# Kernel optimization log

Measured on AMD Instinct MI355X. Metric: run time of the kernel, lower is better.

Reference implementation:

```python
import jax, jax.numpy as jnp
import numpy as np

DIM = 1024
SEQ = 32768
BATCH = 1
MIN_ACTIVE = 0.01
MAX_ACTIVE = 0.1
KMAX = int(MAX_ACTIVE * DIM) + 1  # static upper bound on dynamic k (<= 102)
EPS = 1e-6


def setup_inputs() -> dict:
    key = jax.random.key(0)
    ks = jax.random.split(key, 7)
    h = DIM // 8
    s = 0.02
    return {
        "x": jax.random.normal(ks[0], (BATCH, SEQ, DIM), jnp.float32),
        # complexity_net: Linear(dim, dim//8) -> GELU -> Linear(dim//8, 1) -> Sigmoid
        "w1": jax.random.normal(ks[1], (DIM, h), jnp.float32) * s,
        "b1": jnp.zeros((h,), jnp.float32),
        "w2": jax.random.normal(ks[2], (h, 1), jnp.float32) * s,
        "b2": jnp.zeros((1,), jnp.float32),
        # gate_net: Linear(dim, dim)
        "wg": jax.random.normal(ks[3], (DIM, DIM), jnp.float32) * s,
        "bg": jnp.zeros((DIM,), jnp.float32),
        # running stats (eval mode: used for normalization, not updated)
        "running_mean": jax.random.normal(ks[4], (DIM,), jnp.float32) * 0.1,
        "running_var": jax.random.uniform(ks[5], (DIM,), jnp.float32, minval=0.5, maxval=1.5),
    }


def reference(x, w1, b1, w2, b2, wg, bg, running_mean, running_var):
    # complexity from seq-mean pooled features -> scalar in (0,1)
    pooled = x.mean(axis=1, keepdims=True)                      # (B,1,D)
    hid = jax.nn.gelu(pooled @ w1 + b1, approximate=False)      # torch GELU is exact erf
    complexity = jax.nn.sigmoid(hid @ w2 + b2)                  # (B,1,1)
    active_ratio = MIN_ACTIVE + (MAX_ACTIVE - MIN_ACTIVE) * complexity
    # torch .int() truncates; clamp(min=1). B==1 so k is effectively scalar.
    k = jnp.clip((active_ratio * DIM).astype(jnp.int32), 1, KMAX)  # (B,1,1)

    importance = jnp.abs(x @ wg + bg)                           # (B,S,D)
    importance = (importance - running_mean) / (jnp.sqrt(running_var) + EPS)

    # dynamic-k topk via static-KMAX top_k + threshold at the k-th largest value
    topk_vals, _ = jax.lax.top_k(importance, KMAX)              # (B,S,KMAX)
    idx = jnp.broadcast_to((k - 1).astype(jnp.int32), (x.shape[0], x.shape[1], 1))
    kth = jnp.take_along_axis(topk_vals, idx, axis=-1)          # (B,S,1)
    mask = (importance >= kth).astype(x.dtype)                  # (B,S,D), non-differentiable
    mask = jax.lax.stop_gradient(mask)

    # straight-through combine: forward = x*mask, backward passes grad to all of x
    sparse_x = x * mask + (x - jax.lax.stop_gradient(x)) * (1.0 - mask)

    complexity_mean = complexity.mean()
    active_ratio_mean = active_ratio.mean()
    active_neurons = k.astype(jnp.float32).mean()
    return sparse_x, complexity_mean, active_ratio_mean, active_neurons
```

## Files before the change

kernel.cpp:

```cpp
#include <hip/hip_runtime.h>
#include <cstdint>
#include <cstddef>

#define SEQ 32768
#define DIM 1024
#define HID 128
#define KMAXV 103

using f4 = __attribute__((ext_vector_type(4))) float;
using f2 = __attribute__((ext_vector_type(2))) float;

__global__ __launch_bounds__(256) void pool_partial(const float* __restrict__ x,
                                                    double* __restrict__ part) {
    const int b = blockIdx.x;
    const int t = threadIdx.x;
    const int r0 = b * 128;
    double s0 = 0.0, s1 = 0.0, s2 = 0.0, s3 = 0.0;
    for (int r = 0; r < 128; ++r) {
        const float* row = x + (size_t)(r0 + r) * DIM;
        s0 += (double)row[t];
        s1 += (double)row[t + 256];
        s2 += (double)row[t + 512];
        s3 += (double)row[t + 768];
    }
    double* p = part + (size_t)b * DIM;
    p[t] = s0; p[t + 256] = s1; p[t + 512] = s2; p[t + 768] = s3;
}

__global__ __launch_bounds__(1024) void tiny_net(const double* __restrict__ part,
                                                 const float* __restrict__ w1,
                                                 const float* __restrict__ b1,
                                                 const float* __restrict__ w2,
                                                 const float* __restrict__ b2,
                                                 float* __restrict__ out_scalars,
                                                 int* __restrict__ kout) {
    __shared__ double pooled[DIM];
    __shared__ double hidv[HID];
    const int t = threadIdx.x;

    double s = 0.0;
    for (int b = 0; b < 256; ++b) s += part[(size_t)b * DIM + t];
    pooled[t] = s / (double)SEQ;
    __syncthreads();

    if (t < HID) {
        double h = (double)b1[t];
        for (int d = 0; d < DIM; ++d) h += pooled[d] * (double)w1[d * HID + t];
        h = 0.5 * h * (1.0 + erf(h * 0.70710678118654752440));
        hidv[t] = h;
    }
    __syncthreads();

    if (t == 0) {
        double z = (double)b2[0];
        for (int j = 0; j < HID; ++j) z += hidv[j] * (double)w2[j];
        double c = 1.0 / (1.0 + exp(-z));
        double ar = 0.01 + 0.09 * c;
        int k = (int)(ar * (double)DIM);
        if (k < 1) k = 1;
        if (k > KMAXV) k = KMAXV;
        out_scalars[0] = (float)c;
        out_scalars[1] = (float)ar;
        out_scalars[2] = (float)k;
        *kout = k;
    }
}

#define BM 16
#define CBLOCK 512

template<int K0, int K1>
__device__ __forceinline__ void panel_acc(const float* __restrict__ x,
                                          const float* __restrict__ wbase,
                                          int row0, float pacc[16][2]) {
#pragma unroll
    for (int m = 0; m < 16; ++m) { pacc[m][0] = 0.0f; pacc[m][1] = 0.0f; }

    f2 wc0 = *(const f2*)(wbase + (size_t)(K0 + 0) * DIM);
    f2 wc1 = *(const f2*)(wbase + (size_t)(K0 + 1) * DIM);
    f2 wc2 = *(const f2*)(wbase + (size_t)(K0 + 2) * DIM);
    f2 wc3 = *(const f2*)(wbase + (size_t)(K0 + 3) * DIM);
    f2 wn0 = *(const f2*)(wbase + (size_t)(K0 + 4) * DIM);
    f2 wn1 = *(const f2*)(wbase + (size_t)(K0 + 5) * DIM);
    f2 wn2_ = *(const f2*)(wbase + (size_t)(K0 + 6) * DIM);
    f2 wn3 = *(const f2*)(wbase + (size_t)(K0 + 7) * DIM);

    for (int kk0 = K0; kk0 < K1; kk0 += 4) {
        const int kp = kk0 + 8;
        const int kn2 = (kp < K1) ? kp : K0;
        const f2 p0 = *(const f2*)(wbase + (size_t)(kn2 + 0) * DIM);
        const f2 p1 = *(const f2*)(wbase + (size_t)(kn2 + 1) * DIM);
        const f2 p2 = *(const f2*)(wbase + (size_t)(kn2 + 2) * DIM);
        const f2 p3 = *(const f2*)(wbase + (size_t)(kn2 + 3) * DIM);

        const float* xp = x + (size_t)row0 * DIM + kk0;
#pragma unroll
        for (int m = 0; m < 16; ++m) {
            const f4 xq = *(const f4*)(xp + m * DIM);
            float a0 = pacc[m][0], a1 = pacc[m][1];
            a0 = fmaf(xq[0], wc0[0], a0); a1 = fmaf(xq[0], wc0[1], a1);
            a0 = fmaf(xq[1], wc1[0], a0); a1 = fmaf(xq[1], wc1[1], a1);
            a0 = fmaf(xq[2], wc2[0], a0); a1 = fmaf(xq[2], wc2[1], a1);
            a0 = fmaf(xq[3], wc3[0], a0); a1 = fmaf(xq[3], wc3[1], a1);
            pacc[m][0] = a0; pacc[m][1] = a1;
        }
        wc0 = wn0; wc1 = wn1; wc2 = wn2_; wc3 = wn3;
        wn0 = p0;  wn1 = p1;  wn2_ = p2;  wn3 = p3;
    }
}

__global__ __launch_bounds__(CBLOCK) void panel1_kernel(const float* __restrict__ x,
                                                        const float* __restrict__ wg,
                                                        float* __restrict__ out) {
    const int t = threadIdx.x;
    const int c2 = t << 1;
    const int row0 = blockIdx.x * BM;

    float pacc[16][2];
    panel_acc<0, 384>(x, wg + c2, row0, pacc);

#pragma unroll
    for (int m = 0; m < 16; ++m) {
        f2 v; v[0] = pacc[m][0]; v[1] = pacc[m][1];
        *(f2*)(out + (size_t)(row0 + m) * DIM + c2) = v;
    }
}

__global__ __launch_bounds__(CBLOCK) void panel23_kernel(const float* __restrict__ x,
                                                         const float* __restrict__ wg,
                                                         const float* __restrict__ bg,
                                                         const float* __restrict__ rm,
                                                         const float* __restrict__ rv,
                                                         const int* __restrict__ kptr,
                                                         float* __restrict__ out) {
    __shared__ float lbuf[8 * DIM];

    const int t = threadIdx.x;
    const int c2 = t << 1;
    const int row0 = blockIdx.x * BM;

    float pacc[16][2];

    panel_acc<384, 704>(x, wg + c2, row0, pacc);
    float d12[16][2];
#pragma unroll
    for (int m = 0; m < 16; ++m) {
        const f2 d = *(const f2*)(out + (size_t)(row0 + m) * DIM + c2);
        d12[m][0] = d[0] + pacc[m][0];
        d12[m][1] = d[1] + pacc[m][1];
    }

    panel_acc<704, 1024>(x, wg + c2, row0, pacc);
    float dot[16][2];
#pragma unroll
    for (int m = 0; m < 16; ++m) {
        dot[m][0] = d12[m][0] + pacc[m][0];
        dot[m][1] = d12[m][1] + pacc[m][1];
    }

    const f2 vbg = *(const f2*)(bg + c2);
    const f2 vrm = *(const f2*)(rm + c2);
    const f2 vrv = *(const f2*)(rv + c2);
    f2 vden;
    vden[0] = sqrtf(vrv[0]) + 1e-6f;
    vden[1] = sqrtf(vrv[1]) + 1e-6f;

    f2 imp[16];
#pragma unroll
    for (int m = 0; m < 16; ++m) {
        imp[m][0] = (fabsf(dot[m][0] + vbg[0]) - vrm[0]) / vden[0];
        imp[m][1] = (fabsf(dot[m][1] + vbg[1]) - vrm[1]) / vden[1];
    }

    int kval = *kptr;
    if (kval < 1) kval = 1;
    if (kval > DIM) kval = DIM;

    float (*selbuf)[DIM] = (float (*)[DIM])lbuf;

    for (int ch = 0; ch < 2; ++ch) {
        __syncthreads();
#pragma unroll
        for (int m = 0; m < 8; ++m)
            *(f2*)(&selbuf[m][c2]) = imp[ch * 8 + m];
        __syncthreads();

        const int w = t >> 6;
        const int l = t & 63;
        const size_t srow = (size_t)(row0 + ch * 8 + w);

        unsigned keys[16];
#pragma unroll
        for (int j = 0; j < 4; ++j) {
            const f4 v = *(const f4*)(&selbuf[w][4 * l + 256 * j]);
#pragma unroll
            for (int i = 0; i < 4; ++i) {
                const unsigned u = __float_as_uint(v[i]);
                keys[j * 4 + i] = (u & 0x80000000u) ? ~u : (u | 0x80000000u);
            }
        }

        unsigned pref = 0u;
        for (int b = 31; b >= 0; --b) {
            const unsigned tt = pref | (1u << b);
            int cnt = 0;
#pragma unroll
            for (int j = 0; j < 16; ++j) cnt += (keys[j] >= tt) ? 1 : 0;
#pragma unroll
            for (int off = 32; off >= 1; off >>= 1) cnt += __shfl_xor(cnt, off, 64);
            if (cnt >= kval) pref = tt;
        }

        const float* xr = x + srow * DIM;
        float* orow = out + srow * DIM;
#pragma unroll
        for (int j = 0; j < 4; ++j) {
            const f4 xv = *(const f4*)(xr + 4 * l + 256 * j);
            f4 o;
#pragma unroll
            for (int i = 0; i < 4; ++i) o[i] = (keys[j * 4 + i] >= pref) ? xv[i] : 0.0f;
            *(f4*)(orow + 4 * l + 256 * j) = o;
        }
    }
}

extern "C" void kernel_launch(void* const* d_in, const int* in_sizes, int n_in,
                              void* d_out, int out_size, void* d_ws, size_t ws_size,
                              hipStream_t stream) {
    const float* x  = (const float*)d_in[0];
    const float* w1 = (const float*)d_in[1];
    const float* b1 = (const float*)d_in[2];
    const float* w2 = (const float*)d_in[3];
    const float* b2 = (const float*)d_in[4];
    const float* wg = (const float*)d_in[5];
    const float* bg = (const float*)d_in[6];
    const float* rm = (const float*)d_in[7];
    const float* rv = (const float*)d_in[8];
    float* out = (float*)d_out;

    double* part = (double*)d_ws;
    int* kptr = (int*)((char*)d_ws + (size_t)256 * DIM * sizeof(double));

    pool_partial<<<256, 256, 0, stream>>>(x, part);
    tiny_net<<<1, 1024, 0, stream>>>(part, w1, b1, w2, b2,
                                     out + (size_t)SEQ * DIM, kptr);
    panel1_kernel<<<SEQ / BM, CBLOCK, 0, stream>>>(x, wg, out);
    panel23_kernel<<<SEQ / BM, CBLOCK, 0, stream>>>(x, wg, bg, rm, rv, kptr, out);
}
```

Before: 1.045 ms.

## Use packed FP32 FMA inline asm and split panel kernel into three launches

Replaces scalar fmaf accumulation with v_pk_fma_f32 inline assembly that uses scalar-register x operands broadcast across two output columns, and restructures the weight prefetch into an 8-wide double step. The former combined panel2/3 kernel is split into separate panel2 and panel3 kernels. Panel2 adds its partial into the output buffer, which panel3 then reads back. The packed FMA is meant to halve the FMA instruction count. The split is meant to cut register pressure, which should help occupancy. In exchange it adds a kernel launch and an extra read-modify-write pass over the output.

```diff
diff --git a/kernel.cpp b/kernel.cpp
--- a/kernel.cpp
+++ b/kernel.cpp
@@ -69,43 +69,55 @@
 #define BM 16
 #define CBLOCK 512
 
+__device__ __forceinline__ void fma_step(const float* __restrict__ xp,
+                                         f2 w0, f2 w1, f2 w2, f2 w3,
+                                         f2 acc[16]) {
+#pragma unroll
+    for (int m = 0; m < 16; ++m) {
+        const f2 xab = *(const f2*)(xp + m * DIM);
+        const f2 xcd = *(const f2*)(xp + m * DIM + 2);
+        asm("v_pk_fma_f32 %0, %1, %2, %0 op_sel:[0,0,0] op_sel_hi:[0,1,1]"
+            : "+v"(acc[m]) : "s"(xab), "v"(w0));
+        asm("v_pk_fma_f32 %0, %1, %2, %0 op_sel:[1,0,0] op_sel_hi:[1,1,1]"
+            : "+v"(acc[m]) : "s"(xab), "v"(w1));
+        asm("v_pk_fma_f32 %0, %1, %2, %0 op_sel:[0,0,0] op_sel_hi:[0,1,1]"
+            : "+v"(acc[m]) : "s"(xcd), "v"(w2));
+        asm("v_pk_fma_f32 %0, %1, %2, %0 op_sel:[1,0,0] op_sel_hi:[1,1,1]"
+            : "+v"(acc[m]) : "s"(xcd), "v"(w3));
+    }
+}
+
 template<int K0, int K1>
 __device__ __forceinline__ void panel_acc(const float* __restrict__ x,
                                           const float* __restrict__ wbase,
-                                          int row0, float pacc[16][2]) {
-#pragma unroll
-    for (int m = 0; m < 16; ++m) { pacc[m][0] = 0.0f; pacc[m][1] = 0.0f; }
-
-    f2 wc0 = *(const f2*)(wbase + (size_t)(K0 + 0) * DIM);
-    f2 wc1 = *(const f2*)(wbase + (size_t)(K0 + 1) * DIM);
-    f2 wc2 = *(const f2*)(wbase + (size_t)(K0 + 2) * DIM);
-    f2 wc3 = *(const f2*)(wbase + (size_t)(K0 + 3) * DIM);
-    f2 wn0 = *(const f2*)(wbase + (size_t)(K0 + 4) * DIM);
-    f2 wn1 = *(const f2*)(wbase + (size_t)(K0 + 5) * DIM);
-    f2 wn2_ = *(const f2*)(wbase + (size_t)(K0 + 6) * DIM);
-    f2 wn3 = *(const f2*)(wbase + (size_t)(K0 + 7) * DIM);
-
-    for (int kk0 = K0; kk0 < K1; kk0 += 4) {
-        const int kp = kk0 + 8;
-        const int kn2 = (kp < K1) ? kp : K0;
-        const f2 p0 = *(const f2*)(wbase + (size_t)(kn2 + 0) * DIM);
-        const f2 p1 = *(const f2*)(wbase + (size_t)(kn2 + 1) * DIM);
-        const f2 p2 = *(const f2*)(wbase + (size_t)(kn2 + 2) * DIM);
-        const f2 p3 = *(const f2*)(wbase + (size_t)(kn2 + 3) * DIM);
-
-        const float* xp = x + (size_t)row0 * DIM + kk0;
-#pragma unroll
-        for (int m = 0; m < 16; ++m) {
-            const f4 xq = *(const f4*)(xp + m * DIM);
-            float a0 = pacc[m][0], a1 = pacc[m][1];
-            a0 = fmaf(xq[0], wc0[0], a0); a1 = fmaf(xq[0], wc0[1], a1);
-            a0 = fmaf(xq[1], wc1[0], a0); a1 = fmaf(xq[1], wc1[1], a1);
-            a0 = fmaf(xq[2], wc2[0], a0); a1 = fmaf(xq[2], wc2[1], a1);
-            a0 = fmaf(xq[3], wc3[0], a0); a1 = fmaf(xq[3], wc3[1], a1);
-            pacc[m][0] = a0; pacc[m][1] = a1;
-        }
-        wc0 = wn0; wc1 = wn1; wc2 = wn2_; wc3 = wn3;
-        wn0 = p0;  wn1 = p1;  wn2_ = p2;  wn3 = p3;
+                                          int row0, f2 acc[16]) {
+#pragma unroll
+    for (int m = 0; m < 16; ++m) { acc[m][0] = 0.0f; acc[m][1] = 0.0f; }
+
+    const float* xbase = x + (size_t)row0 * DIM;
+
+    f2 a0 = *(const f2*)(wbase + (size_t)(K0 + 0) * DIM);
+    f2 a1 = *(const f2*)(wbase + (size_t)(K0 + 1) * DIM);
+    f2 a2 = *(const f2*)(wbase + (size_t)(K0 + 2) * DIM);
+    f2 a3 = *(const f2*)(wbase + (size_t)(K0 + 3) * DIM);
+
+    for (int kk0 = K0; kk0 < K1; kk0 += 8) {
+        const f2 b0 = *(const f2*)(wbase + (size_t)(kk0 + 4) * DIM);
+        const f2 b1 = *(const f2*)(wbase + (size_t)(kk0 + 5) * DIM);
+        const f2 b2v = *(const f2*)(wbase + (size_t)(kk0 + 6) * DIM);
+        const f2 b3 = *(const f2*)(wbase + (size_t)(kk0 + 7) * DIM);
+
+        fma_step(xbase + kk0, a0, a1, a2, a3, acc);
+
+        const int kn = (kk0 + 8 < K1) ? kk0 + 8 : K0;
+        const f2 c0 = *(const f2*)(wbase + (size_t)(kn + 0) * DIM);
+        const f2 c1 = *(const f2*)(wbase + (size_t)(kn + 1) * DIM);
+        const f2 c2v = *(const f2*)(wbase + (size_t)(kn + 2) * DIM);
+        const f2 c3 = *(const f2*)(wbase + (size_t)(kn + 3) * DIM);
+
+        fma_step(xbase + kk0 + 4, b0, b1, b2v, b3, acc);
+
+        a0 = c0; a1 = c1; a2 = c2v; a3 = c3;
     }
 }
 
@@ -116,46 +128,56 @@
     const int c2 = t << 1;
     const int row0 = blockIdx.x * BM;
 
-    float pacc[16][2];
+    f2 pacc[16];
     panel_acc<0, 384>(x, wg + c2, row0, pacc);
 
 #pragma unroll
-    for (int m = 0; m < 16; ++m) {
-        f2 v; v[0] = pacc[m][0]; v[1] = pacc[m][1];
-        *(f2*)(out + (size_t)(row0 + m) * DIM + c2) = v;
-    }
-}
-
-__global__ __launch_bounds__(CBLOCK) void panel23_kernel(const float* __restrict__ x,
-                                                         const float* __restrict__ wg,
-                                                         const float* __restrict__ bg,
-                                                         const float* __restrict__ rm,
-                                                         const float* __restrict__ rv,
-                                                         const int* __restrict__ kptr,
-                                                         float* __restrict__ out) {
-    __shared__ float lbuf[8 * DIM];
-
+    for (int m = 0; m < 16; ++m)
+        *(f2*)(out + (size_t)(row0 + m) * DIM + c2) = pacc[m];
+}
+
+__global__ __launch_bounds__(CBLOCK) void panel2_kernel(const float* __restrict__ x,
+                                                        const float* __restrict__ wg,
+                                                        float* __restrict__ out) {
     const int t = threadIdx.x;
     const int c2 = t << 1;
     const int row0 = blockIdx.x * BM;
 
-    float pacc[16][2];
-
+    f2 pacc[16];
     panel_acc<384, 704>(x, wg + c2, row0, pacc);
-    float d12[16][2];
+
+#pragma unroll
+    for (int m = 0; m < 16; ++m) {
+        float* op = out + (size_t)(row0 + m) * DIM + c2;
+        f2 d = *(const f2*)op;
+        d[0] = d[0] + pacc[m][0];
+        d[1] = d[1] + pacc[m][1];
+        *(f2*)op = d;
+    }
+}
+
+__global__ __launch_bounds__(CBLOCK) void panel3_kernel(const float* __restrict__ x,
+                                                        const float* __restrict__ wg,
+                                                        const float* __restrict__ bg,
+                                                        const float* __restrict__ rm,
+                                                        const float* __restrict__ rv,
+                                                        const int* __restrict__ kptr,
+                                                        float* __restrict__ out) {
+    __shared__ float lbuf[8 * DIM];
+
+    const int t = threadIdx.x;
+    const int c2 = t << 1;
+    const int row0 = blockIdx.x * BM;
+
+    f2 pacc[16];
+    panel_acc<704, 1024>(x, wg + c2, row0, pacc);
+
+    float dot[16][2];
 #pragma unroll
     for (int m = 0; m < 16; ++m) {
         const f2 d = *(const f2*)(out + (size_t)(row0 + m) * DIM + c2);
-        d12[m][0] = d[0] + pacc[m][0];
-        d12[m][1] = d[1] + pacc[m][1];
-    }
-
-    panel_acc<704, 1024>(x, wg + c2, row0, pacc);
-    float dot[16][2];
-#pragma unroll
-    for (int m = 0; m < 16; ++m) {
-        dot[m][0] = d12[m][0] + pacc[m][0];
-        dot[m][1] = d12[m][1] + pacc[m][1];
+        dot[m][0] = d[0] + pacc[m][0];
+        dot[m][1] = d[1] + pacc[m][1];
     }
 
     const f2 vbg = *(const f2*)(bg + c2);
@@ -245,5 +267,6 @@
     tiny_net<<<1, 1024, 0, stream>>>(part, w1, b1, w2, b2,
                                      out + (size_t)SEQ * DIM, kptr);
     panel1_kernel<<<SEQ / BM, CBLOCK, 0, stream>>>(x, wg, out);
-    panel23_kernel<<<SEQ / BM, CBLOCK, 0, stream>>>(x, wg, bg, rm, rv, kptr, out);
-}
+    panel2_kernel<<<SEQ / BM, CBLOCK, 0, stream>>>(x, wg, out);
+    panel3_kernel<<<SEQ / BM, CBLOCK, 0, stream>>>(x, wg, bg, rm, rv, kptr, out);
+}
```

After: 0.9999 ms. 1.05x faster.
